# Kernel optimization log

Measured on AMD Instinct MI355X. Metric: run time of the kernel, lower is better.

The kernel has to match this reference:

```python
import heapq
import jax, jax.numpy as jnp
import numpy as np

NB_CLASSES = 50257
INPUT_DIM = 512
BATCH = 1024
NB_REQ = 8


def build_huffman(nb_classes):
    """Replicates Huffmax.build: huffman tree over equal frequencies,
    codes padded with 0, paths padded with root node id."""
    heap = [(1, i, i) for i in range(nb_classes)]  # (freq, tiebreak, payload)
    heapq.heapify(heap)
    node_id = 0
    tiebreak = nb_classes
    while len(heap) > 1:
        f1, _, left = heapq.heappop(heap)
        f2, _, right = heapq.heappop(heap)
        heapq.heappush(heap, (f1 + f2, tiebreak, ('n', node_id, left, right)))
        node_id += 1
        tiebreak += 1
    root = heap[0][2]
    total_nodes = node_id  # = nb_classes - 1
    root_id = root[1]
    codes, paths = {}, {}
    stack = [(root, [], [])]
    while stack:
        node, code, path = stack.pop()
        if isinstance(node, tuple):
            _, nid, l, r = node
            stack.append((l, code + [0], path + [nid]))
            stack.append((r, code + [1], path + [nid]))
        else:
            codes[node] = code
            paths[node] = path
    max_depth = max(len(c) for c in codes.values())
    code_arr = np.zeros((nb_classes, max_depth), np.float32)
    path_arr = np.full((nb_classes, max_depth), root_id, np.int32)
    for c in range(nb_classes):
        code_arr[c, :len(codes[c])] = codes[c]
        path_arr[c, :len(paths[c])] = paths[c]
    return code_arr, path_arr, total_nodes


def setup_inputs() -> dict:
    key = jax.random.key(0)
    k1, k2, k3 = jax.random.split(key, 3)
    code_arr, path_arr, total_nodes = build_huffman(NB_CLASSES)
    input_vector = jax.random.normal(k1, (BATCH, INPUT_DIM), dtype=jnp.float32)
    target_classes = jax.random.randint(k2, (BATCH, NB_REQ), 0, NB_CLASSES, dtype=jnp.int32)
    # glorot-ish scaled node weights (original W is (total_nodes, input_dim, 1))
    W = jax.random.normal(k3, (total_nodes, INPUT_DIM), dtype=jnp.float32) * (1.0 / np.sqrt(INPUT_DIM))
    b = jnp.zeros((total_nodes,), dtype=jnp.float32)
    return {
        'input_vector': input_vector,
        'target_classes': target_classes,
        'W': W,
        'b': b,
        'class_paths': jnp.asarray(path_arr),
        'huffman_codes': jnp.asarray(code_arr),
    }


def reference(input_vector, target_classes, W, b, class_paths, huffman_codes):
    # req_nodes: (B, R, D) node ids along huffman path for each requested class
    req_nodes = class_paths[target_classes]
    # req_W: (B, R, D, I) gathered node weight rows; y = x . W_node + b_node
    req_W = W[req_nodes]
    y = jnp.einsum('bi,brdi->brd', input_vector, req_W) + b[req_nodes]
    y = jax.nn.sigmoid(y)
    codes = huffman_codes[target_classes]  # (B, R, D) in {0,1} (0-padded)
    # factor = y if code==0 else (1-y); product along the path
    return jnp.prod(codes + y - 2.0 * codes * y, axis=-1)
```

## Files before the change

### kernel.cpp

```cpp
#include <hip/hip_runtime.h>
#include <math.h>

#define WPB 4

template<int CTRL, int ROW_MASK>
__device__ __forceinline__ float dpp_add(float v) {
    const int s = __builtin_amdgcn_update_dpp(0, __float_as_int(v),
                                              CTRL, ROW_MASK, 0xf, false);
    return v + __int_as_float(s);
}

__device__ __forceinline__ float wave_sum63(float v) {
    v = dpp_add<0x111, 0xf>(v);
    v = dpp_add<0x112, 0xf>(v);
    v = dpp_add<0x114, 0xf>(v);
    v = dpp_add<0x118, 0xf>(v);
    v = dpp_add<0x142, 0xa>(v);
    v = dpp_add<0x143, 0xc>(v);
    return v;
}

__device__ __forceinline__ float readlane_f(float v, int lane) {
    return __int_as_float(__builtin_amdgcn_readlane(__float_as_int(v), lane));
}

template<int D>
__global__ __launch_bounds__(WPB * 64, 4)
void huff_kernel(const float* __restrict__ x,
                 const int*   __restrict__ tgt,
                 const float* __restrict__ W,
                 const float* __restrict__ bias,
                 const int*   __restrict__ paths,
                 const float* __restrict__ codes,
                 float*       __restrict__ out,
                 int R, int I, int npairs)
{
    const int lane = threadIdx.x & 63;
    const int p    = blockIdx.x * WPB + (threadIdx.x >> 6);
    if (p >= npairs) return;
    const int b = p / R;

    const float4* xrow = reinterpret_cast<const float4*>(x + (size_t)b * I);
    const float4 xa = xrow[lane];
    const float4 xb = xrow[lane + 64];

    const int c  = tgt[p];
    const int dd = (lane < D) ? lane : (D - 1);
    const int   nd = paths[(size_t)c * D + dd];
    const float cd = codes[(size_t)c * D + dd];
    const float sd = 1.0f - 2.0f * cd;
    const float bv = bias[nd];

    float acc[D];
    #pragma unroll
    for (int d = 0; d < D; ++d) {
        const int node = readlane_f(__int_as_float(nd), d) == 0.0f ? 0 : 0; (void)node;
        const int nid  = __builtin_amdgcn_readlane(nd, d);
        const float4* wr = reinterpret_cast<const float4*>(W + (size_t)nid * I);
        const float4 wa = wr[lane];
        const float4 wb = wr[lane + 64];
        acc[d] = xa.x * wa.x + xa.y * wa.y + xa.z * wa.z + xa.w * wa.w
               + xb.x * wb.x + xb.y * wb.y + xb.z * wb.z + xb.w * wb.w;
    }

    #pragma unroll
    for (int d = 0; d < D; ++d) acc[d] = wave_sum63(acc[d]);

    float q = 1.0f;
    #pragma unroll
    for (int d = 0; d < D; ++d) {
        const float tot = readlane_f(acc[d], 63);
        const float bb  = readlane_f(bv, d);
        const float ss  = readlane_f(sd, d);
        q *= 1.0f + __expf(-ss * (tot + bb));
    }
    if (lane == 0) out[p] = 1.0f / q;
}

__global__ __launch_bounds__(WPB * 64)
void huff_kernel_gen(const float* __restrict__ x, const int* __restrict__ tgt,
                     const float* __restrict__ W, const float* __restrict__ bias,
                     const int* __restrict__ paths, const float* __restrict__ codes,
                     float* __restrict__ out, int R, int I, int D, int npairs)
{
    const int lane = threadIdx.x & 63;
    const int p = blockIdx.x * WPB + (threadIdx.x >> 6);
    if (p >= npairs) return;
    const int b = p / R;
    const float4* xrow = reinterpret_cast<const float4*>(x + (size_t)b * I);
    const float4 xa = xrow[lane];
    const float4 xb = xrow[lane + 64];
    const int c = tgt[p];
    float q = 1.0f;
    for (int d = 0; d < D; ++d) {
        const int node = paths[(size_t)c * D + d];
        const float4* wr = reinterpret_cast<const float4*>(W + (size_t)node * I);
        const float4 wa = wr[lane];
        const float4 wb = wr[lane + 64];
        float acc = xa.x * wa.x + xa.y * wa.y + xa.z * wa.z + xa.w * wa.w
                  + xb.x * wb.x + xb.y * wb.y + xb.z * wb.z + xb.w * wb.w;
        #pragma unroll
        for (int off = 32; off; off >>= 1) acc += __shfl_xor(acc, off, 64);
        const float t = acc + bias[node];
        const float s = 1.0f - 2.0f * codes[(size_t)c * D + d];
        q *= 1.0f + __expf(-s * t);
    }
    if (lane == 0) out[p] = 1.0f / q;
}

extern "C" void kernel_launch(void* const* d_in, const int* in_sizes, int n_in,
                              void* d_out, int out_size, void* d_ws, size_t ws_size,
                              hipStream_t stream) {
    const float* x     = (const float*)d_in[0];
    const int*   tgt   = (const int*)  d_in[1];
    const float* W     = (const float*)d_in[2];
    const float* bias  = (const float*)d_in[3];
    const int*   paths = (const int*)  d_in[4];
    const float* codes = (const float*)d_in[5];
    float* out = (float*)d_out;

    const int N = in_sizes[3];
    const int C = N + 1;
    const int I = in_sizes[2] / N;
    const int B = in_sizes[0] / I;
    const int R = in_sizes[1] / B;
    const int D = in_sizes[4] / C;

    const int npairs = B * R;
    const int grid = (npairs + WPB - 1) / WPB;

    switch (D) {
    case 15: huff_kernel<15><<<grid, WPB * 64, 0, stream>>>(x, tgt, W, bias, paths, codes, out, R, I, npairs); break;
    case 16: huff_kernel<16><<<grid, WPB * 64, 0, stream>>>(x, tgt, W, bias, paths, codes, out, R, I, npairs); break;
    case 17: huff_kernel<17><<<grid, WPB * 64, 0, stream>>>(x, tgt, W, bias, paths, codes, out, R, I, npairs); break;
    case 18: huff_kernel<18><<<grid, WPB * 64, 0, stream>>>(x, tgt, W, bias, paths, codes, out, R, I, npairs); break;
    default: huff_kernel_gen<<<grid, WPB * 64, 0, stream>>>(x, tgt, W, bias, paths, codes, out, R, I, D, npairs); break;
    }
}
```

Measured before the change: 24.33 us.

## Split each pair's Huffman path across two waves and combine via shared memory

Each (batch, request) pair's 16-node path is now split across two wavefronts, with 8 nodes per wave. The two partial products are combined through shared memory after a block barrier. Halving the serial gather and reduce chain per wave doubles the number of waves, which is meant to expose more memory-level parallelism on the gathered W rows. The cost is that the x row is loaded twice and a __syncthreads is added, and the specialised path is limited to D==16 and I==512.

New measurement: 24.12 us. About the same (-0.9%).

```diff
diff --git a/kernel.cpp b/kernel.cpp
--- a/kernel.cpp
+++ b/kernel.cpp
@@ -1,7 +1,5 @@
 #include <hip/hip_runtime.h>
 #include <math.h>
-
-#define WPB 4
 
 template<int CTRL, int ROW_MASK>
 __device__ __forceinline__ float dpp_add(float v) {
@@ -20,42 +18,39 @@
     return v;
 }
 
-__device__ __forceinline__ float readlane_f(float v, int lane) {
-    return __int_as_float(__builtin_amdgcn_readlane(__float_as_int(v), lane));
+__device__ __forceinline__ float readlane_f(float v, int l) {
+    return __int_as_float(__builtin_amdgcn_readlane(__float_as_int(v), l));
 }
 
-template<int D>
-__global__ __launch_bounds__(WPB * 64, 4)
-void huff_kernel(const float* __restrict__ x,
-                 const int*   __restrict__ tgt,
-                 const float* __restrict__ W,
-                 const float* __restrict__ bias,
-                 const int*   __restrict__ paths,
-                 const float* __restrict__ codes,
-                 float*       __restrict__ out,
-                 int R, int I, int npairs)
+__global__ __launch_bounds__(256, 4)
+void huff_half(const float* __restrict__ x, const int* __restrict__ tgt,
+               const float* __restrict__ W, const float* __restrict__ bias,
+               const int* __restrict__ paths, const float* __restrict__ codes,
+               float* __restrict__ out, int R, int I)
 {
+    __shared__ float qsh[2][2];
     const int lane = threadIdx.x & 63;
-    const int p    = blockIdx.x * WPB + (threadIdx.x >> 6);
-    if (p >= npairs) return;
-    const int b = p / R;
+    const int w    = threadIdx.x >> 6;
+    const int pi   = w >> 1;
+    const int h    = w & 1;
+    const int p    = blockIdx.x * 2 + pi;
+    const int b    = p / R;
 
     const float4* xrow = reinterpret_cast<const float4*>(x + (size_t)b * I);
     const float4 xa = xrow[lane];
     const float4 xb = xrow[lane + 64];
 
-    const int c  = tgt[p];
-    const int dd = (lane < D) ? lane : (D - 1);
-    const int   nd = paths[(size_t)c * D + dd];
-    const float cd = codes[(size_t)c * D + dd];
+    const int c     = tgt[p];
+    const int dglob = h * 8 + (lane & 7);
+    const int   nd = paths[(size_t)c * 16 + dglob];
+    const float cd = codes[(size_t)c * 16 + dglob];
     const float sd = 1.0f - 2.0f * cd;
     const float bv = bias[nd];
 
-    float acc[D];
+    float acc[8];
     #pragma unroll
-    for (int d = 0; d < D; ++d) {
-        const int node = readlane_f(__int_as_float(nd), d) == 0.0f ? 0 : 0; (void)node;
-        const int nid  = __builtin_amdgcn_readlane(nd, d);
+    for (int d = 0; d < 8; ++d) {
+        const int nid = __builtin_amdgcn_readlane(nd, d);
         const float4* wr = reinterpret_cast<const float4*>(W + (size_t)nid * I);
         const float4 wa = wr[lane];
         const float4 wb = wr[lane + 64];
@@ -64,27 +59,29 @@
     }
 
     #pragma unroll
-    for (int d = 0; d < D; ++d) acc[d] = wave_sum63(acc[d]);
+    for (int d = 0; d < 8; ++d) acc[d] = wave_sum63(acc[d]);
 
     float q = 1.0f;
     #pragma unroll
-    for (int d = 0; d < D; ++d) {
+    for (int d = 0; d < 8; ++d) {
         const float tot = readlane_f(acc[d], 63);
         const float bb  = readlane_f(bv, d);
         const float ss  = readlane_f(sd, d);
         q *= 1.0f + __expf(-ss * (tot + bb));
     }
-    if (lane == 0) out[p] = 1.0f / q;
+    if (lane == 0) qsh[pi][h] = q;
+    __syncthreads();
+    if (h == 0 && lane == 0) out[p] = 1.0f / (qsh[pi][0] * qsh[pi][1]);
 }
 
-__global__ __launch_bounds__(WPB * 64)
+__global__ __launch_bounds__(256)
 void huff_kernel_gen(const float* __restrict__ x, const int* __restrict__ tgt,
                      const float* __restrict__ W, const float* __restrict__ bias,
                      const int* __restrict__ paths, const float* __restrict__ codes,
                      float* __restrict__ out, int R, int I, int D, int npairs)
 {
     const int lane = threadIdx.x & 63;
-    const int p = blockIdx.x * WPB + (threadIdx.x >> 6);
+    const int p = blockIdx.x * 4 + (threadIdx.x >> 6);
     if (p >= npairs) return;
     const int b = p / R;
     const float4* xrow = reinterpret_cast<const float4*>(x + (size_t)b * I);
@@ -127,13 +124,13 @@
     const int D = in_sizes[4] / C;
 
     const int npairs = B * R;
-    const int grid = (npairs + WPB - 1) / WPB;
 
-    switch (D) {
-    case 15: huff_kernel<15><<<grid, WPB * 64, 0, stream>>>(x, tgt, W, bias, paths, codes, out, R, I, npairs); break;
-    case 16: huff_kernel<16><<<grid, WPB * 64, 0, stream>>>(x, tgt, W, bias, paths, codes, out, R, I, npairs); break;
-    case 17: huff_kernel<17><<<grid, WPB * 64, 0, stream>>>(x, tgt, W, bias, paths, codes, out, R, I, npairs); break;
-    case 18: huff_kernel<18><<<grid, WPB * 64, 0, stream>>>(x, tgt, W, bias, paths, codes, out, R, I, npairs); break;
-    default: huff_kernel_gen<<<grid, WPB * 64, 0, stream>>>(x, tgt, W, bias, paths, codes, out, R, I, D, npairs); break;
+    if (D == 16 && I == 512 && (npairs & 1) == 0) {
+        huff_half<<<npairs / 2, 256, 0, stream>>>(x, tgt, W, bias, paths, codes,
+                                                  out, R, I);
+    } else {
+        const int grid = (npairs + 3) / 4;
+        huff_kernel_gen<<<grid, 256, 0, stream>>>(x, tgt, W, bias, paths, codes,
+                                                  out, R, I, D, npairs);
     }
 }
```
